# Optimization experiments

Measured on AMD Instinct MI355X. Metric: run time of the kernel, lower is better.

## Reference

```python
import jax, jax.numpy as jnp
import numpy as np

IN_DIM, OUT_DIM = 256, 64
ALPHA = 0.2  # leaky relu negative slope
NEG_INF = -1e30


def setup_inputs() -> dict:
    key = jax.random.key(0)
    k1, k2, k3, k4 = jax.random.split(key, 4)
    B, N = 8, 2048
    h = jax.random.normal(k1, (B, N, IN_DIM), dtype=jnp.float32)
    adj = jax.random.randint(k2, (B, N, N), 0, 2, dtype=jnp.int32)
    # ensure no fully-isolated node (avoids softmax over all -inf)
    idx = jnp.arange(N)
    adj = adj.at[:, idx, idx].set(1)
    # params: fc.weight [out,in] -> store transposed [in,out]; attn_fc.weight [1, 2*out] -> [2*out]
    W = jax.random.normal(k3, (IN_DIM, OUT_DIM), dtype=jnp.float32) / np.sqrt(IN_DIM)
    a = jax.random.normal(k4, (2 * OUT_DIM,), dtype=jnp.float32) / np.sqrt(2 * OUT_DIM)
    return {"h": h, "adj": adj, "W": W, "a": a}


def reference(h, adj, W, a):
    # Wh: [B,N,D]
    Wh = jnp.einsum("bni,io->bno", h, W)
    D = Wh.shape[-1]
    # concat-based additive attention decomposed: e[b,i,j] = lrelu(a1.Wh_i + a2.Wh_j)
    a1, a2 = a[:D], a[D:]
    s1 = Wh @ a1  # [B,N] contribution of row node i
    s2 = Wh @ a2  # [B,N] contribution of col node j
    e = jax.nn.leaky_relu(s1[:, :, None] + s2[:, None, :], negative_slope=ALPHA)  # [B,N,N]
    e = jnp.where(adj == 0, NEG_INF, e)
    attn = jax.nn.softmax(e, axis=-1)
    # dropout is identity in eval mode
    return jnp.einsum("bij,bjd->bid", attn, Wh)
```

## Files before the change

kernel.cpp:

```cpp
#include <hip/hip_runtime.h>
#include <math.h>

#define NB 8
#define NN 2048
#define IN_DIM 256
#define OUT_DIM 64
#define ALPHA 0.2f
#define JSPLIT 8

typedef __attribute__((ext_vector_type(8))) short bf16x8;
typedef __attribute__((ext_vector_type(4))) float f32x4;
typedef __attribute__((ext_vector_type(4))) int   i32x4;

__device__ __forceinline__ unsigned short f2bf(float x) {
    union { float f; unsigned u; } v; v.f = x;
    unsigned r = v.u + 0x7FFF + ((v.u >> 16) & 1);
    return (unsigned short)(r >> 16);
}
__device__ __forceinline__ float bf2f(unsigned short b) {
    union { unsigned u; float f; } v; v.u = ((unsigned)b) << 16;
    return v.f;
}

#define WT_STRIDE 264
__global__ __launch_bounds__(256) void wh_kernel(const float* __restrict__ h,
                                                 const float* __restrict__ W,
                                                 const float* __restrict__ a,
                                                 unsigned short* __restrict__ Whbt,
                                                 float* __restrict__ s1,
                                                 float* __restrict__ s2) {
    __shared__ unsigned short Wt[OUT_DIM * WT_STRIDE];
    const int t = threadIdx.x;

    #pragma unroll 8
    for (int rep = 0; rep < 64; ++rep) {
        const int id = rep * 256 + t;
        const int k = id >> 6, n = id & 63;
        Wt[n * WT_STRIDE + k] = f2bf(W[id]);
    }
    __syncthreads();

    const int lane = t & 63, wv = t >> 6;
    const int m = lane & 15, quad = lane >> 4;
    const long gr0 = (long)(blockIdx.x * 4 + wv) * 16;

    f32x4 acc[4];
    #pragma unroll
    for (int nt = 0; nt < 4; ++nt) acc[nt] = (f32x4){0.f, 0.f, 0.f, 0.f};

    #pragma unroll
    for (int ks = 0; ks < 8; ++ks) {
        const int k0 = ks * 32;
        const float* hp = h + (gr0 + m) * IN_DIM + k0 + quad * 8;
        const float4 ha = *(const float4*)hp;
        const float4 hb = *(const float4*)(hp + 4);
        bf16x8 af;
        af[0] = (short)f2bf(ha.x); af[1] = (short)f2bf(ha.y);
        af[2] = (short)f2bf(ha.z); af[3] = (short)f2bf(ha.w);
        af[4] = (short)f2bf(hb.x); af[5] = (short)f2bf(hb.y);
        af[6] = (short)f2bf(hb.z); af[7] = (short)f2bf(hb.w);
        #pragma unroll
        for (int nt = 0; nt < 4; ++nt) {
            const bf16x8 bf_ = *(const bf16x8*)(const void*)
                &Wt[(nt * 16 + m) * WT_STRIDE + k0 + quad * 8];
            acc[nt] = __builtin_amdgcn_mfma_f32_16x16x32_bf16(af, bf_, acc[nt], 0, 0, 0);
        }
    }

    const int b  = (int)(gr0 >> 11);
    const int ib = (int)(gr0 & 2047);

    #pragma unroll
    for (int nt = 0; nt < 4; ++nt) {
        ushort4 w4;
        w4.x = f2bf(acc[nt][0]); w4.y = f2bf(acc[nt][1]);
        w4.z = f2bf(acc[nt][2]); w4.w = f2bf(acc[nt][3]);
        *(ushort4*)&Whbt[((long)(b * OUT_DIM + nt * 16 + m) << 11) + ib + quad * 4] = w4;
    }

    float a1v[4], a2v[4];
    #pragma unroll
    for (int nt = 0; nt < 4; ++nt) {
        a1v[nt] = a[nt * 16 + m];
        a2v[nt] = a[OUT_DIM + nt * 16 + m];
    }
    #pragma unroll
    for (int reg = 0; reg < 4; ++reg) {
        float p1 = 0.f, p2 = 0.f;
        #pragma unroll
        for (int nt = 0; nt < 4; ++nt) {
            p1 += acc[nt][reg] * a1v[nt];
            p2 += acc[nt][reg] * a2v[nt];
        }
        #pragma unroll
        for (int off = 1; off < 16; off <<= 1) {
            p1 += __shfl_xor(p1, off, 64);
            p2 += __shfl_xor(p2, off, 64);
        }
        if (m == 0) {
            s1[gr0 + quad * 4 + reg] = p1;
            s2[gr0 + quad * 4 + reg] = p2;
        }
    }
}

__device__ __forceinline__ float pcalc(int av, float s2e, float s1v) {
    float e = s1v + s2e;
    e = e > 0.f ? e : ALPHA * e;
    const float p = __expf(e);
    return av != 0 ? p : 0.f;
}

__global__ __launch_bounds__(256) void attn_kernel(const int* __restrict__ adj,
                                                   const unsigned short* __restrict__ Whbt,
                                                   const float* __restrict__ s1,
                                                   const float* __restrict__ s2,
                                                   float* __restrict__ part,
                                                   float* __restrict__ lpart) {
    const int t = threadIdx.x, lane = t & 63, wv = t >> 6;
    const int bid = blockIdx.x;
    const int js  = bid & (JSPLIT - 1);
    const int itg = (bid >> 3) & 31;
    const int b   = bid >> 8;
    const int i0  = itg * 64 + wv * 16;
    const int jlo = js * (NN / JSPLIT);

    const int m = lane & 15, quad = lane >> 4;

    const int*   adjp = adj + (long)b * NN * NN + (long)(i0 + m) * NN + jlo + quad * 8;
    const float* s2p  = s2 + b * NN + jlo + quad * 8;
    const unsigned short* wbase = Whbt + ((long)(b * OUT_DIM) << 11) + jlo + quad * 8;
    const float s1v = s1[b * NN + i0 + m];

    f32x4 acc[4];
    #pragma unroll
    for (int nt = 0; nt < 4; ++nt) acc[nt] = (f32x4){0.f, 0.f, 0.f, 0.f};
    float lsum = 0.f;

    i32x4  av0 = __builtin_nontemporal_load((const i32x4*)adjp);
    i32x4  av1 = __builtin_nontemporal_load((const i32x4*)(adjp + 4));
    float4 sv0 = *(const float4*)s2p;
    float4 sv1 = *(const float4*)(s2p + 4);

    #pragma unroll
    for (int ks = 0; ks < NN / JSPLIT / 32; ++ks) {
        const int j0 = ks * 32;

        bf16x8 bfr[4];
        #pragma unroll
        for (int nt = 0; nt < 4; ++nt)
            bfr[nt] = *(const bf16x8*)(const void*)
                &wbase[(((long)(nt * 16 + m)) << 11) + j0];

        const i32x4  ca0 = av0, ca1 = av1;
        const float4 cs0 = sv0, cs1 = sv1;
        if (ks < NN / JSPLIT / 32 - 1) {
            av0 = __builtin_nontemporal_load((const i32x4*)(adjp + j0 + 32));
            av1 = __builtin_nontemporal_load((const i32x4*)(adjp + j0 + 36));
            sv0 = *(const float4*)(s2p + j0 + 32);
            sv1 = *(const float4*)(s2p + j0 + 36);
        }

        float pv[8];
        pv[0] = pcalc(ca0.x, cs0.x, s1v); pv[1] = pcalc(ca0.y, cs0.y, s1v);
        pv[2] = pcalc(ca0.z, cs0.z, s1v); pv[3] = pcalc(ca0.w, cs0.w, s1v);
        pv[4] = pcalc(ca1.x, cs1.x, s1v); pv[5] = pcalc(ca1.y, cs1.y, s1v);
        pv[6] = pcalc(ca1.z, cs1.z, s1v); pv[7] = pcalc(ca1.w, cs1.w, s1v);

        bf16x8 af;
        #pragma unroll
        for (int e = 0; e < 8; ++e) {
            const unsigned short bb = f2bf(pv[e]);
            af[e] = (short)bb;
            lsum += bf2f(bb);
        }

        #pragma unroll
        for (int nt = 0; nt < 4; ++nt)
            acc[nt] = __builtin_amdgcn_mfma_f32_16x16x32_bf16(af, bfr[nt], acc[nt], 0, 0, 0);
    }

    lsum += __shfl_xor(lsum, 16, 64);
    lsum += __shfl_xor(lsum, 32, 64);
    if (quad == 0)
        lpart[js * (NB * NN) + b * NN + i0 + m] = lsum;

    float* pp = part + (long)js * ((long)NB * NN * OUT_DIM)
                     + ((long)(b * NN + i0) << 6);
    #pragma unroll
    for (int nt = 0; nt < 4; ++nt)
        #pragma unroll
        for (int reg = 0; reg < 4; ++reg)
            pp[(quad * 4 + reg) * OUT_DIM + nt * 16 + m] = acc[nt][reg];
}

__global__ __launch_bounds__(256) void finalize_kernel(const float* __restrict__ part,
                                                       const float* __restrict__ lpart,
                                                       float* __restrict__ out) {
    const int idx = blockIdx.x * 256 + threadIdx.x;
    const int row = idx >> 4;
    float l = 0.f;
    #pragma unroll
    for (int s = 0; s < JSPLIT; ++s) l += lpart[s * (NB * NN) + row];
    float4 v = make_float4(0.f, 0.f, 0.f, 0.f);
    const float4* p4 = (const float4*)part;
    #pragma unroll
    for (int s = 0; s < JSPLIT; ++s) {
        const float4 p = p4[(long)s * ((long)NB * NN * OUT_DIM / 4) + idx];
        v.x += p.x; v.y += p.y; v.z += p.z; v.w += p.w;
    }
    const float inv = 1.f / l;
    v.x *= inv; v.y *= inv; v.z *= inv; v.w *= inv;
    ((float4*)out)[idx] = v;
}

extern "C" void kernel_launch(void* const* d_in, const int* in_sizes, int n_in,
                              void* d_out, int out_size, void* d_ws, size_t ws_size,
                              hipStream_t stream) {
    const float* h   = (const float*)d_in[0];
    const int*   adj = (const int*)d_in[1];
    const float* W   = (const float*)d_in[2];
    const float* a   = (const float*)d_in[3];
    float* out = (float*)d_out;

    float* s1    = (float*)d_ws;
    float* s2    = s1 + NB * NN;
    float* lpart = s2 + NB * NN;
    float* part  = lpart + JSPLIT * NB * NN;
    unsigned short* Whbt =
        (unsigned short*)(part + (long)JSPLIT * NB * NN * OUT_DIM);

    wh_kernel<<<NB * NN / 64, 256, 0, stream>>>(h, W, a, Whbt, s1, s2);
    attn_kernel<<<NB * (NN / 64) * JSPLIT, 256, 0, stream>>>(adj, Whbt, s1, s2, part, lpart);
    finalize_kernel<<<NB * NN * OUT_DIM / 4 / 256, 256, 0, stream>>>(part, lpart, out);
}
```

Before: 244.1 us.

## Halve j-split, deepen adj prefetch, compute row sums with MFMA ones-vector

Reduces JSPLIT from 8 to 4 so each attention block covers 512 columns, halving the partial-sum traffic that finalize has to read. The adj/s2 prefetch becomes a two-deep ring so loads are issued two iterations ahead. The scalar per-lane row-sum accumulation with bf16 round-trips is replaced by an extra MFMA against a vector of bf16 ones, moving the normalizer onto the matrix unit. It also adds an occupancy hint of 4 blocks per CU. The cost is fewer blocks, less parallelism, and a longer serial loop per block.

```diff
diff --git a/kernel.cpp b/kernel.cpp
--- a/kernel.cpp
+++ b/kernel.cpp
@@ -6,7 +6,7 @@
 #define IN_DIM 256
 #define OUT_DIM 64
 #define ALPHA 0.2f
-#define JSPLIT 8
+#define JSPLIT 4
 
 typedef __attribute__((ext_vector_type(8))) short bf16x8;
 typedef __attribute__((ext_vector_type(4))) float f32x4;
@@ -16,10 +16,6 @@
     union { float f; unsigned u; } v; v.f = x;
     unsigned r = v.u + 0x7FFF + ((v.u >> 16) & 1);
     return (unsigned short)(r >> 16);
-}
-__device__ __forceinline__ float bf2f(unsigned short b) {
-    union { unsigned u; float f; } v; v.u = ((unsigned)b) << 16;
-    return v.f;
 }
 
 #define WT_STRIDE 264
@@ -111,17 +107,17 @@
     return av != 0 ? p : 0.f;
 }
 
-__global__ __launch_bounds__(256) void attn_kernel(const int* __restrict__ adj,
-                                                   const unsigned short* __restrict__ Whbt,
-                                                   const float* __restrict__ s1,
-                                                   const float* __restrict__ s2,
-                                                   float* __restrict__ part,
-                                                   float* __restrict__ lpart) {
+__global__ __launch_bounds__(256, 4) void attn_kernel(const int* __restrict__ adj,
+                                                      const unsigned short* __restrict__ Whbt,
+                                                      const float* __restrict__ s1,
+                                                      const float* __restrict__ s2,
+                                                      float* __restrict__ part,
+                                                      float* __restrict__ lpart) {
     const int t = threadIdx.x, lane = t & 63, wv = t >> 6;
     const int bid = blockIdx.x;
     const int js  = bid & (JSPLIT - 1);
-    const int itg = (bid >> 3) & 31;
-    const int b   = bid >> 8;
+    const int itg = (bid >> 2) & 31;
+    const int b   = bid >> 7;
     const int i0  = itg * 64 + wv * 16;
     const int jlo = js * (NN / JSPLIT);
 
@@ -135,16 +131,26 @@
     f32x4 acc[4];
     #pragma unroll
     for (int nt = 0; nt < 4; ++nt) acc[nt] = (f32x4){0.f, 0.f, 0.f, 0.f};
-    float lsum = 0.f;
-
-    i32x4  av0 = __builtin_nontemporal_load((const i32x4*)adjp);
-    i32x4  av1 = __builtin_nontemporal_load((const i32x4*)(adjp + 4));
-    float4 sv0 = *(const float4*)s2p;
-    float4 sv1 = *(const float4*)(s2p + 4);
-
-    #pragma unroll
-    for (int ks = 0; ks < NN / JSPLIT / 32; ++ks) {
+    f32x4 racc = (f32x4){0.f, 0.f, 0.f, 0.f};
+
+    bf16x8 bones;
+    #pragma unroll
+    for (int e = 0; e < 8; ++e) bones[e] = (short)0x3F80;
+
+    i32x4  av0[2], av1[2];
+    float4 sv0[2], sv1[2];
+    #pragma unroll
+    for (int p = 0; p < 2; ++p) {
+        av0[p] = __builtin_nontemporal_load((const i32x4*)(adjp + p * 32));
+        av1[p] = __builtin_nontemporal_load((const i32x4*)(adjp + p * 32 + 4));
+        sv0[p] = *(const float4*)(s2p + p * 32);
+        sv1[p] = *(const float4*)(s2p + p * 32 + 4);
+    }
+
+    #pragma unroll 2
+    for (int ks = 0; ks < 16; ++ks) {
         const int j0 = ks * 32;
+        const int cur = ks & 1;
 
         bf16x8 bfr[4];
         #pragma unroll
@@ -152,13 +158,13 @@
             bfr[nt] = *(const bf16x8*)(const void*)
                 &wbase[(((long)(nt * 16 + m)) << 11) + j0];
 
-        const i32x4  ca0 = av0, ca1 = av1;
-        const float4 cs0 = sv0, cs1 = sv1;
-        if (ks < NN / JSPLIT / 32 - 1) {
-            av0 = __builtin_nontemporal_load((const i32x4*)(adjp + j0 + 32));
-            av1 = __builtin_nontemporal_load((const i32x4*)(adjp + j0 + 36));
-            sv0 = *(const float4*)(s2p + j0 + 32);
-            sv1 = *(const float4*)(s2p + j0 + 36);
+        const i32x4  ca0 = av0[cur], ca1 = av1[cur];
+        const float4 cs0 = sv0[cur], cs1 = sv1[cur];
+        if (ks < 14) {
+            av0[cur] = __builtin_nontemporal_load((const i32x4*)(adjp + j0 + 64));
+            av1[cur] = __builtin_nontemporal_load((const i32x4*)(adjp + j0 + 68));
+            sv0[cur] = *(const float4*)(s2p + j0 + 64);
+            sv1[cur] = *(const float4*)(s2p + j0 + 68);
         }
 
         float pv[8];
@@ -169,21 +175,19 @@
 
         bf16x8 af;
         #pragma unroll
-        for (int e = 0; e < 8; ++e) {
-            const unsigned short bb = f2bf(pv[e]);
-            af[e] = (short)bb;
-            lsum += bf2f(bb);
-        }
+        for (int e = 0; e < 8; ++e) af[e] = (short)f2bf(pv[e]);
 
         #pragma unroll
         for (int nt = 0; nt < 4; ++nt)
             acc[nt] = __builtin_amdgcn_mfma_f32_16x16x32_bf16(af, bfr[nt], acc[nt], 0, 0, 0);
-    }
-
-    lsum += __shfl_xor(lsum, 16, 64);
-    lsum += __shfl_xor(lsum, 32, 64);
-    if (quad == 0)
-        lpart[js * (NB * NN) + b * NN + i0 + m] = lsum;
+        racc = __builtin_amdgcn_mfma_f32_16x16x32_bf16(af, bones, racc, 0, 0, 0);
+    }
+
+    if (m == 0) {
+        #pragma unroll
+        for (int reg = 0; reg < 4; ++reg)
+            lpart[js * (NB * NN) + b * NN + i0 + quad * 4 + reg] = racc[reg];
+    }
 
     float* pp = part + (long)js * ((long)NB * NN * OUT_DIM)
                      + ((long)(b * NN + i0) << 6);
```

Result: faster. 235.7 us (-3.4%).
